# Kernel optimization log

Hardware: AMD Instinct MI355X
Metric: run time of the kernel (lower is better)

Reference implementation:

```python
import jax, jax.numpy as jnp
import numpy as np

H = 64
V = 50257
B = 32
L = 4096
LN_EPS = 1e-5
DELTA_EPS = 1e-6


def setup_inputs() -> dict:
    key = jax.random.key(0)
    ks = jax.random.split(key, 10)
    s = 0.02
    return {
        "seq": jax.random.randint(ks[0], (B, L), 0, V),
        "read_pos": -1,
        "embed": jax.random.normal(ks[1], (V, H), jnp.float32) * s,
        "w1": jax.random.normal(ks[2], (H, 2 * H), jnp.float32) * s,
        "b1": jnp.zeros((2 * H,), jnp.float32),
        "w2": jax.random.normal(ks[3], (2 * H, H), jnp.float32) * s,
        "b2": jnp.zeros((H,), jnp.float32),
        "ln_g": jnp.ones((H,), jnp.float32),
        "ln_b": jnp.zeros((H,), jnp.float32),
        "rp_w": jax.random.normal(ks[4], (H, H), jnp.float32) * s,
        "rp_b": jnp.zeros((H,), jnp.float32),
        "out_w": jax.random.normal(ks[5], (H, V), jnp.float32) * s,
        "out_b": jnp.zeros((V,), jnp.float32),
    }


def _encoder(seq, embed, w1, b1, w2, b2, ln_g, ln_b):
    e = embed[seq]  # [B, L, H]
    f = jnp.maximum(e @ w1 + b1, 0.0) @ w2 + b2  # FFN
    x = e + f
    mu = jnp.mean(x, axis=-1, keepdims=True)
    var = jnp.mean((x - mu) ** 2, axis=-1, keepdims=True)
    return (x - mu) * jax.lax.rsqrt(var + LN_EPS) * ln_g + ln_b


def _delta_memory(h_all):
    # Strictly sequential delta-rule fast-weight update over t = 0..L-2.
    Bs, Ls, Hs = h_all.shape
    keys = jnp.transpose(h_all[:, : Ls - 1, :], (1, 0, 2))  # [L-1, B, H]

    def step(M, k):
        vp = jnp.einsum('bij,bj->bi', M, k)  # M @ k
        u = k - vp / (jnp.sum(k * k, axis=-1, keepdims=True) + DELTA_EPS)
        M = M + u[:, :, None] * k[:, None, :]  # outer product update
        return M, None

    M0 = jnp.zeros((Bs, Hs, Hs), h_all.dtype)
    M, _ = jax.lax.scan(step, M0, keys)
    return M


def reference(seq, read_pos, embed, w1, b1, w2, b2, ln_g, ln_b, rp_w, rp_b, out_w, out_b):
    h_all = _encoder(seq, embed, w1, b1, w2, b2, ln_g, ln_b)  # [B, L, H]
    M = _delta_memory(h_all)  # [B, H, H]
    q = h_all[:, read_pos, :]  # [B, H]
    r = jnp.einsum('bij,bj->bi', M, q)
    return (r @ rp_w + rp_b) @ out_w + out_b  # [B, V]
```

## Files before the change

### kernel.cpp

```cpp
#include <hip/hip_runtime.h>

#define HH 64
#define VV 50257
#define BB 32
#define LL 4096

constexpr float LN_EPS_F = 1e-5f;
constexpr float DELTA_EPS_F = 1e-6f;

constexpr int CS = 64;
constexpr int NG = LL / CS;

typedef float f32x4 __attribute__((ext_vector_type(4)));
typedef short bf16x8 __attribute__((ext_vector_type(8)));
union U16x8 { uint4 u; bf16x8 v; unsigned short s[8]; };

__device__ __forceinline__ unsigned short f2bf(float f) {
  union { float f; unsigned u; } v; v.f = f;
  unsigned r = v.u + 0x7fff + ((v.u >> 16) & 1);
  return (unsigned short)(r >> 16);
}

template <int CTRL>
__device__ __forceinline__ float dpp_add(float x) {
  int t = __builtin_amdgcn_update_dpp(0, __float_as_int(x), CTRL, 0xF, 0xF, true);
  return x + __int_as_float(t);
}

__device__ __forceinline__ float wave_sum_lane63(float x) {
  x = dpp_add<0x111>(x);
  x = dpp_add<0x112>(x);
  x = dpp_add<0x114>(x);
  x = dpp_add<0x118>(x);
  x = dpp_add<0x142>(x);
  x = dpp_add<0x143>(x);
  return x;
}

__device__ __forceinline__ float readlane_f(float x, int lane) {
  return __int_as_float(__builtin_amdgcn_readlane(__float_as_int(x), lane));
}

__global__ __launch_bounds__(256) void prep_kernel(
    const float* __restrict__ w1, const float* __restrict__ w2,
    unsigned short* __restrict__ w1b, unsigned short* __restrict__ w2b) {
  int i = blockIdx.x * 256 + threadIdx.x;
  if (i < 8192) {
    int jj = i >> 6, h = i & 63;
    w1b[i] = f2bf(w1[h * 128 + jj]);
  } else {
    int k = i - 8192;
    int h = k >> 7, jj = k & 127;
    w2b[k] = f2bf(w2[jj * 64 + h]);
  }
}

__global__ __launch_bounds__(64, 1) void encoder_kernel(
    const int* __restrict__ seq, const float* __restrict__ embed,
    const unsigned short* __restrict__ w1b, const float* __restrict__ b1,
    const unsigned short* __restrict__ w2b, const float* __restrict__ b2,
    const float* __restrict__ ln_g, const float* __restrict__ ln_b,
    float* __restrict__ h_all, float* __restrict__ beta) {
  __shared__ __align__(16) char pool[26624];
  unsigned short (*e_l)[72] = reinterpret_cast<unsigned short (*)[72]>(pool);
  unsigned short (*act_l)[136] = reinterpret_cast<unsigned short (*)[136]>(pool + 9216);
  float (*x_l)[65] = reinterpret_cast<float (*)[65]>(pool);
  __shared__ float2 gb_l[64];
  __shared__ float b1_l[128], b2_l[64];

  int lane = threadIdx.x;
  int q = lane >> 4, l = lane & 15;
  int base = blockIdx.x * 64;
  int s = seq[base + lane];

  {
    const float4* ep = reinterpret_cast<const float4*>(embed + (size_t)s * HH);
#pragma unroll
    for (int i = 0; i < 8; ++i) {
      float4 va = ep[2 * i], vb = ep[2 * i + 1];
      uint4 u;
      u.x = (unsigned)f2bf(va.x) | ((unsigned)f2bf(va.y) << 16);
      u.y = (unsigned)f2bf(va.z) | ((unsigned)f2bf(va.w) << 16);
      u.z = (unsigned)f2bf(vb.x) | ((unsigned)f2bf(vb.y) << 16);
      u.w = (unsigned)f2bf(vb.z) | ((unsigned)f2bf(vb.w) << 16);
      *(uint4*)&e_l[lane][8 * i] = u;
    }
  }
  gb_l[lane] = make_float2(ln_g[lane], ln_b[lane]);
  b1_l[lane] = b1[lane];
  b1_l[64 + lane] = b1[64 + lane];
  b2_l[lane] = b2[lane];

  bf16x8 af1[8][2];
#pragma unroll
  for (int mi = 0; mi < 8; ++mi)
#pragma unroll
    for (int ks = 0; ks < 2; ++ks) {
      U16x8 t;
      t.u = *(const uint4*)(w1b + (mi * 16 + l) * 64 + ks * 32 + q * 8);
      af1[mi][ks] = t.v;
    }

  __syncthreads();

  f32x4 acc1[8][4];
#pragma unroll
  for (int mi = 0; mi < 8; ++mi)
#pragma unroll
    for (int nt = 0; nt < 4; ++nt) acc1[mi][nt] = (f32x4){0.f, 0.f, 0.f, 0.f};

#pragma unroll
  for (int ks = 0; ks < 2; ++ks) {
    bf16x8 bfr[4];
#pragma unroll
    for (int nt = 0; nt < 4; ++nt) {
      U16x8 t;
      t.u = *(const uint4*)&e_l[nt * 16 + l][ks * 32 + q * 8];
      bfr[nt] = t.v;
    }
#pragma unroll
    for (int mi = 0; mi < 8; ++mi)
#pragma unroll
      for (int nt = 0; nt < 4; ++nt)
        acc1[mi][nt] = __builtin_amdgcn_mfma_f32_16x16x32_bf16(
            af1[mi][ks], bfr[nt], acc1[mi][nt], 0, 0, 0);
  }

#pragma unroll
  for (int mi = 0; mi < 8; ++mi)
#pragma unroll
    for (int nt = 0; nt < 4; ++nt) {
      int tok = nt * 16 + l;
      int jj0 = mi * 16 + q * 4;
      float v0 = fmaxf(acc1[mi][nt][0] + b1_l[jj0 + 0], 0.f);
      float v1 = fmaxf(acc1[mi][nt][1] + b1_l[jj0 + 1], 0.f);
      float v2 = fmaxf(acc1[mi][nt][2] + b1_l[jj0 + 2], 0.f);
      float v3 = fmaxf(acc1[mi][nt][3] + b1_l[jj0 + 3], 0.f);
      uint2 u;
      u.x = (unsigned)f2bf(v0) | ((unsigned)f2bf(v1) << 16);
      u.y = (unsigned)f2bf(v2) | ((unsigned)f2bf(v3) << 16);
      *(uint2*)&act_l[tok][jj0] = u;
    }

  bf16x8 bf2[4][4];
#pragma unroll
  for (int nt = 0; nt < 4; ++nt)
#pragma unroll
    for (int ks = 0; ks < 4; ++ks) {
      U16x8 t;
      t.u = *(const uint4*)(w2b + (nt * 16 + l) * 128 + ks * 32 + q * 8);
      bf2[nt][ks] = t.v;
    }

  __syncthreads();

  f32x4 acc2[4][4];
#pragma unroll
  for (int mt = 0; mt < 4; ++mt)
#pragma unroll
    for (int nt = 0; nt < 4; ++nt) acc2[mt][nt] = (f32x4){0.f, 0.f, 0.f, 0.f};

#pragma unroll
  for (int ks = 0; ks < 4; ++ks) {
    bf16x8 afr[4];
#pragma unroll
    for (int mt = 0; mt < 4; ++mt) {
      U16x8 t;
      t.u = *(const uint4*)&act_l[mt * 16 + l][ks * 32 + q * 8];
      afr[mt] = t.v;
    }
#pragma unroll
    for (int mt = 0; mt < 4; ++mt)
#pragma unroll
      for (int nt = 0; nt < 4; ++nt)
        acc2[mt][nt] = __builtin_amdgcn_mfma_f32_16x16x32_bf16(
            afr[mt], bf2[nt][ks], acc2[mt][nt], 0, 0, 0);
  }

  __syncthreads();

#pragma unroll
  for (int mt = 0; mt < 4; ++mt)
#pragma unroll
    for (int nt = 0; nt < 4; ++nt) {
      int h = nt * 16 + l;
#pragma unroll
      for (int r = 0; r < 4; ++r) {
        int tok = mt * 16 + q * 4 + r;
        x_l[tok][h] = acc2[mt][nt][r] + b2_l[h];
      }
    }

  __syncthreads();

  float x[HH];
#pragma unroll
  for (int h = 0; h < HH; ++h) x[h] = x_l[lane][h];
  {
    const float4* ep = reinterpret_cast<const float4*>(embed + (size_t)s * HH);
#pragma unroll
    for (int i = 0; i < 16; ++i) {
      float4 v = ep[i];
      x[4 * i + 0] += v.x; x[4 * i + 1] += v.y;
      x[4 * i + 2] += v.z; x[4 * i + 3] += v.w;
    }
  }
  float sum = 0.f;
#pragma unroll
  for (int h = 0; h < HH; ++h) sum += x[h];
  float mu = sum * (1.f / HH);
  float vs = 0.f;
#pragma unroll
  for (int h = 0; h < HH; ++h) { float dx = x[h] - mu; vs = fmaf(dx, dx, vs); }
  float rstd = rsqrtf(vs * (1.f / HH) + LN_EPS_F);

  float ss = 0.f;
#pragma unroll
  for (int h = 0; h < HH; ++h) {
    float2 gb = gb_l[h];
    float o = fmaf((x[h] - mu) * rstd, gb.x, gb.y);
    ss = fmaf(o, o, ss);
    x[h] = o;
  }
  float4* hp = reinterpret_cast<float4*>(h_all + (size_t)(base + lane) * HH);
#pragma unroll
  for (int i = 0; i < 16; ++i)
    hp[i] = make_float4(x[4 * i + 0], x[4 * i + 1], x[4 * i + 2], x[4 * i + 3]);
  beta[base + lane] = 1.f / (ss + DELTA_EPS_F);
}

__global__ __launch_bounds__(64, 1) void gram_n_kernel(
    const float* __restrict__ h_all, const float* __restrict__ beta,
    float* __restrict__ Ng) {
  __shared__ __align__(16) char smem[37120];
  unsigned short (*pA)[64][72] = reinterpret_cast<unsigned short (*)[64][72]>(smem);
  unsigned short (*pB)[64][72] = reinterpret_cast<unsigned short (*)[64][72]>(smem + 18432);
  float (*Gl)[68] = reinterpret_cast<float (*)[68]>(smem + 18432);
  float* bl = reinterpret_cast<float*>(smem + 36864);

  int c = blockIdx.x, b = blockIdx.y, lane = threadIdx.x;
  int q = lane >> 4, l = lane & 15;
  const float* src = h_all + ((size_t)b * LL + c * CS) * HH;

#pragma unroll
  for (int i = 0; i < 16; ++i) {
    int row = i * 4 + q;
    float4 v = *(const float4*)&src[row * 64 + l * 4];
    float f[4] = {v.x, v.y, v.z, v.w};
    unsigned hs[4], ls[4];
#pragma unroll
    for (int r = 0; r < 4; ++r) {
      unsigned short hb = f2bf(f[r]);
      float hf = __uint_as_float(((unsigned)hb) << 16);
      hs[r] = hb; ls[r] = f2bf(f[r] - hf);
    }
    *(uint2*)&pA[0][row][l * 4] = make_uint2(hs[0] | (hs[1] << 16), hs[2] | (hs[3] << 16));
    *(uint2*)&pA[1][row][l * 4] = make_uint2(ls[0] | (ls[1] << 16), ls[2] | (ls[3] << 16));
  }
  bl[lane] = beta[(size_t)b * LL + c * CS + lane];
  if (c == NG - 1) { pA[0][63][lane] = 0; pA[1][63][lane] = 0; }
  __syncthreads();

  f32x4 acc[4][4];
#pragma unroll
  for (int mi = 0; mi < 4; ++mi)
#pragma unroll
    for (int nt = 0; nt < 4; ++nt) acc[mi][nt] = (f32x4){0.f, 0.f, 0.f, 0.f};

#pragma unroll
  for (int ks = 0; ks < 2; ++ks) {
    bf16x8 ah[4], al_[4];
#pragma unroll
    for (int i = 0; i < 4; ++i) {
      U16x8 t;
      t.u = *(const uint4*)&pA[0][i * 16 + l][ks * 32 + q * 8]; ah[i] = t.v;
      t.u = *(const uint4*)&pA[1][i * 16 + l][ks * 32 + q * 8]; al_[i] = t.v;
    }
#pragma unroll
    for (int mi = 0; mi < 4; ++mi)
#pragma unroll
      for (int nt = 0; nt < 4; ++nt) {
        acc[mi][nt] = __builtin_amdgcn_mfma_f32_16x16x32_bf16(ah[mi], ah[nt], acc[mi][nt], 0, 0, 0);
        acc[mi][nt] = __builtin_amdgcn_mfma_f32_16x16x32_bf16(ah[mi], al_[nt], acc[mi][nt], 0, 0, 0);
        acc[mi][nt] = __builtin_amdgcn_mfma_f32_16x16x32_bf16(al_[mi], ah[nt], acc[mi][nt], 0, 0, 0);
      }
  }

#pragma unroll
  for (int mi = 0; mi < 4; ++mi) {
    int s0 = mi * 16 + q * 4;
    float4 b4 = *(const float4*)&bl[s0];
#pragma unroll
    for (int nt = 0; nt < 4; ++nt) {
      int t = nt * 16 + l;
      Gl[s0 + 0][t] = acc[mi][nt][0] * b4.x;
      Gl[s0 + 1][t] = acc[mi][nt][1] * b4.y;
      Gl[s0 + 2][t] = acc[mi][nt][2] * b4.z;
      Gl[s0 + 3][t] = acc[mi][nt][3] * b4.w;
    }
  }
  __syncthreads();

  float m[64];
#pragma unroll
  for (int t = 0; t < 64; ++t) m[t] = src[t * 64 + lane];
  if (c == NG - 1) m[63] = 0.f;

#pragma unroll
  for (int i = 0; i < 32; ++i) {
    float v0 = m[2 * i], v1 = m[2 * i + 1];
    unsigned short h0 = f2bf(v0), h1 = f2bf(v1);
    float r0 = v0 - __uint_as_float(((unsigned)h0) << 16);
    float r1 = v1 - __uint_as_float(((unsigned)h1) << 16);
    *(unsigned*)&pA[0][lane][2 * i] = (unsigned)h0 | (((unsigned)h1) << 16);
    *(unsigned*)&pA[1][lane][2 * i] = (unsigned)f2bf(r0) | (((unsigned)f2bf(r1)) << 16);
  }

#pragma unroll
  for (int s = 63; s >= 1; --s) {
    float ms = m[s];
    const float* g = &Gl[s][0];
#pragma unroll
    for (int i = 0; i + 3 < s; i += 4) {
      float4 g4 = *(const float4*)(g + i);
      m[i + 0] = fmaf(-g4.x, ms, m[i + 0]);
      m[i + 1] = fmaf(-g4.y, ms, m[i + 1]);
      m[i + 2] = fmaf(-g4.z, ms, m[i + 2]);
      m[i + 3] = fmaf(-g4.w, ms, m[i + 3]);
    }
    for (int t = s & ~3; t < s; ++t) m[t] = fmaf(-g[t], ms, m[t]);
  }

  __syncthreads();

#pragma unroll
  for (int i = 0; i < 32; ++i) {
    float v0 = bl[2 * i] * m[2 * i];
    float v1 = bl[2 * i + 1] * m[2 * i + 1];
    unsigned short h0 = f2bf(v0), h1 = f2bf(v1);
    float r0 = v0 - __uint_as_float(((unsigned)h0) << 16);
    float r1 = v1 - __uint_as_float(((unsigned)h1) << 16);
    *(unsigned*)&pB[0][lane][2 * i] = (unsigned)h0 | (((unsigned)h1) << 16);
    *(unsigned*)&pB[1][lane][2 * i] = (unsigned)f2bf(r0) | (((unsigned)f2bf(r1)) << 16);
  }
  __syncthreads();

  f32x4 acc2[4][4];
#pragma unroll
  for (int mi = 0; mi < 4; ++mi)
#pragma unroll
    for (int nt = 0; nt < 4; ++nt) acc2[mi][nt] = (f32x4){0.f, 0.f, 0.f, 0.f};

#pragma unroll
  for (int ks = 0; ks < 2; ++ks) {
    bf16x8 ah[4], al_[4], bh[4], blo[4];
#pragma unroll
    for (int i = 0; i < 4; ++i) {
      U16x8 t;
      t.u = *(const uint4*)&pA[0][i * 16 + l][ks * 32 + q * 8]; ah[i] = t.v;
      t.u = *(const uint4*)&pA[1][i * 16 + l][ks * 32 + q * 8]; al_[i] = t.v;
      t.u = *(const uint4*)&pB[0][i * 16 + l][ks * 32 + q * 8]; bh[i] = t.v;
      t.u = *(const uint4*)&pB[1][i * 16 + l][ks * 32 + q * 8]; blo[i] = t.v;
    }
#pragma unroll
    for (int mi = 0; mi < 4; ++mi)
#pragma unroll
      for (int nt = 0; nt < 4; ++nt) {
        acc2[mi][nt] = __builtin_amdgcn_mfma_f32_16x16x32_bf16(ah[mi], bh[nt], acc2[mi][nt], 0, 0, 0);
        acc2[mi][nt] = __builtin_amdgcn_mfma_f32_16x16x32_bf16(ah[mi], blo[nt], acc2[mi][nt], 0, 0, 0);
        acc2[mi][nt] = __builtin_amdgcn_mfma_f32_16x16x32_bf16(al_[mi], bh[nt], acc2[mi][nt], 0, 0, 0);
      }
  }

  float* np = Ng + (((size_t)b * NG + c) << 12);
#pragma unroll
  for (int mi = 0; mi < 4; ++mi)
#pragma unroll
    for (int nt = 0; nt < 4; ++nt) {
      int h0 = mi * 16 + q * 4, hp = nt * 16 + l;
      float4 v;
      v.x = ((h0 + 0 == hp) ? 1.f : 0.f) - acc2[mi][nt][0];
      v.y = ((h0 + 1 == hp) ? 1.f : 0.f) - acc2[mi][nt][1];
      v.z = ((h0 + 2 == hp) ? 1.f : 0.f) - acc2[mi][nt][2];
      v.w = ((h0 + 3 == hp) ? 1.f : 0.f) - acc2[mi][nt][3];
      *(float4*)&np[hp * 64 + h0] = v;
    }
}

__global__ __launch_bounds__(64, 1) void boundary_kernel(
    const float* __restrict__ h_all, const float* __restrict__ Ng,
    const int* __restrict__ read_pos_p, float* __restrict__ Qg) {
  __shared__ __align__(16) float nt0[64 * 64];
  __shared__ __align__(16) float nt1[64 * 64];
  __shared__ __align__(16) float ql[64];

  int b = blockIdx.x, lane = threadIdx.x;
  int rpv = read_pos_p[0];
  int pos = rpv < 0 ? rpv + LL : rpv;
  float Q = h_all[((size_t)b * LL + pos) * HH + lane];

  const float* Nb = Ng + ((size_t)b * NG << 12);

  auto load_chunk = [&](float* buf, int c) {
    const float* g = Nb + ((size_t)c << 12);
#pragma unroll
    for (int i = 0; i < 16; ++i)
      __builtin_amdgcn_global_load_lds(
          (const __attribute__((address_space(1))) unsigned*)(g + i * 256 + lane * 4),
          (__attribute__((address_space(3))) unsigned*)(buf + i * 256), 16, 0, 0);
  };

  auto step = [&](const float* buf, int c, bool last) {
    if (last) __builtin_amdgcn_s_waitcnt(0x0F70);
    else      __builtin_amdgcn_s_waitcnt(0x4F70);
    Qg[((size_t)b * NG + c) * HH + lane] = Q;
    ql[lane] = Q;
    float a0 = 0.f, a1 = 0.f, a2 = 0.f, a3 = 0.f;
#pragma unroll
    for (int j = 0; j < 64; j += 4) {
      float4 q4 = *(const float4*)&ql[j];
      a0 = fmaf(buf[(j + 0) * 64 + lane], q4.x, a0);
      a1 = fmaf(buf[(j + 1) * 64 + lane], q4.y, a1);
      a2 = fmaf(buf[(j + 2) * 64 + lane], q4.z, a2);
      a3 = fmaf(buf[(j + 3) * 64 + lane], q4.w, a3);
    }
    Q = (a0 + a1) + (a2 + a3);
  };

  load_chunk(nt1, NG - 1);
  load_chunk(nt0, NG - 2);

#pragma unroll 1
  for (int c = NG - 1; c >= 1; c -= 2) {
    step(nt1, c, false);
    __builtin_amdgcn_s_waitcnt(0xC07F);
    if (c >= 3) load_chunk(nt1, c - 2);
    step(nt0, c - 1, c == 1);
    __builtin_amdgcn_s_waitcnt(0xC07F);
    if (c >= 3) load_chunk(nt0, c - 3);
  }
}

__global__ __launch_bounds__(64, 1) void chunk_scan_kernel(
    const float* __restrict__ h_all, const float* __restrict__ beta,
    const float* __restrict__ Qg, float* __restrict__ rc) {
  int c = blockIdx.x, b = blockIdx.y, j = threadIdx.x;
  const float* hb = h_all + (size_t)b * LL * HH;
  const float* betab = beta + (size_t)b * LL;

  float P = Qg[((size_t)b * NG + c) * HH + j];
  float r = 0.f;

  float kk[CS];
#pragma unroll
  for (int i = 0; i < CS; ++i) kk[i] = hb[((size_t)(c * CS + i)) * HH + j];
  float bv = betab[c * CS + j];

  bool last = (c == NG - 1);
#pragma unroll
  for (int i = CS - 1; i >= 0; --i) {
    float k = kk[i];
    float bt = readlane_f(bv, i);
    float m = k * P;
    float s = wave_sum_lane63(m);
    float d = readlane_f(s, 63);
    if (i == CS - 1 && last) d = 0.f;
    r = fmaf(d, k, r);
    P = fmaf(-(bt * d), k, P);
  }
  rc[((size_t)b * NG + c) * HH + j] = r;
}

__global__ __launch_bounds__(64, 1) void combine_kernel(
    const float* __restrict__ rc, const float* __restrict__ rp_w,
    const float* __restrict__ rp_b, float* __restrict__ yv) {
  int b = blockIdx.x, j = threadIdx.x;
  float r = 0.f;
#pragma unroll 8
  for (int cc = 0; cc < NG; ++cc) r += rc[((size_t)b * NG + cc) * HH + j];
  __shared__ float rs[HH];
  rs[j] = r;
  __syncthreads();
  float yj = rp_b[j];
#pragma unroll
  for (int h = 0; h < HH; ++h) yj = fmaf(rs[h], rp_w[h * HH + j], yj);
  yv[b * HH + j] = yj;
}

__global__ __launch_bounds__(256, 2) void out_kernel(
    const float* __restrict__ yv, const float* __restrict__ out_w,
    const float* __restrict__ out_b, float* __restrict__ out) {
  __shared__ float ys[BB * HH];
  for (int i = threadIdx.x; i < BB * HH; i += 256) ys[i] = yv[i];
  __syncthreads();

  int v = blockIdx.x * 256 + threadIdx.x;
  if (v >= VV) return;

  float acc[BB];
  float ob = out_b[v];
#pragma unroll
  for (int b = 0; b < BB; ++b) acc[b] = ob;

  for (int h = 0; h < HH; ++h) {
    float w = out_w[(size_t)h * VV + v];
#pragma unroll
    for (int b = 0; b < BB; ++b) acc[b] = fmaf(ys[b * HH + h], w, acc[b]);
  }
#pragma unroll
  for (int b = 0; b < BB; ++b) out[(size_t)b * VV + v] = acc[b];
}

extern "C" void kernel_launch(void* const* d_in, const int* in_sizes, int n_in,
                              void* d_out, int out_size, void* d_ws, size_t ws_size,
                              hipStream_t stream) {
  (void)in_sizes; (void)n_in; (void)out_size; (void)ws_size;
  const int*   seq   = (const int*)d_in[0];
  const int*   rp    = (const int*)d_in[1];
  const float* embed = (const float*)d_in[2];
  const float* w1    = (const float*)d_in[3];
  const float* b1    = (const float*)d_in[4];
  const float* w2    = (const float*)d_in[5];
  const float* b2    = (const float*)d_in[6];
  const float* ln_g  = (const float*)d_in[7];
  const float* ln_b  = (const float*)d_in[8];
  const float* rp_w  = (const float*)d_in[9];
  const float* rp_b  = (const float*)d_in[10];
  const float* out_w = (const float*)d_in[11];
  const float* out_b = (const float*)d_in[12];
  float* out = (float*)d_out;

  float* h_all = (float*)d_ws;
  float* beta  = h_all + (size_t)BB * LL * HH;
  float* Ng    = beta + (size_t)BB * LL;
  float* Qg    = Ng + (size_t)BB * NG * HH * HH;
  float* rcv   = Qg + (size_t)BB * NG * HH;
  float* yv    = rcv + (size_t)BB * NG * HH;
  unsigned short* w1b = (unsigned short*)(yv + (size_t)BB * HH);
  unsigned short* w2b = w1b + 8192;

  prep_kernel<<<64, 256, 0, stream>>>(w1, w2, w1b, w2b);
  encoder_kernel<<<BB * LL / 64, 64, 0, stream>>>(seq, embed, w1b, b1, w2b, b2,
                                                  ln_g, ln_b, h_all, beta);
  gram_n_kernel<<<dim3(NG, BB), 64, 0, stream>>>(h_all, beta, Ng);
  boundary_kernel<<<BB, 64, 0, stream>>>(h_all, Ng, rp, Qg);
  chunk_scan_kernel<<<dim3(NG, BB), 64, 0, stream>>>(h_all, beta, Qg, rcv);
  combine_kernel<<<BB, 64, 0, stream>>>(rcv, rp_w, rp_b, yv);
  out_kernel<<<(VV + 255) / 256, 256, 0, stream>>>(yv, out_w, out_b, out);
}
```

Measured before the change: 234.9 us.

## Pack lower-triangular Gram in LDS and block the chunk triangular solve

The Gram matrix is now computed only for lower-triangular tiles and stored packed (strict lower part), with beta scaling folded into a 4x4-blocked back-substitution that reuses each loaded row group for four updates. The second matmul is split into four passes over 16-column slices so the B operand buffer shrinks, reducing LDS footprint and MFMA count. This trades simpler indexing for more complex packed addressing and a manual waitcnt between per-quarter writes and reads, which carries a synchronization risk.

```diff
diff --git a/kernel.cpp b/kernel.cpp
--- a/kernel.cpp
+++ b/kernel.cpp
@@ -232,11 +232,11 @@
 __global__ __launch_bounds__(64, 1) void gram_n_kernel(
     const float* __restrict__ h_all, const float* __restrict__ beta,
     float* __restrict__ Ng) {
-  __shared__ __align__(16) char smem[37120];
+  __shared__ __align__(16) char smem[27136];
   unsigned short (*pA)[64][72] = reinterpret_cast<unsigned short (*)[64][72]>(smem);
-  unsigned short (*pB)[64][72] = reinterpret_cast<unsigned short (*)[64][72]>(smem + 18432);
-  float (*Gl)[68] = reinterpret_cast<float (*)[68]>(smem + 18432);
-  float* bl = reinterpret_cast<float*>(smem + 36864);
+  float* Glp = reinterpret_cast<float*>(smem + 18432);
+  unsigned short (*pBq)[16][72] = reinterpret_cast<unsigned short (*)[16][72]>(smem + 18432);
+  float* bl = reinterpret_cast<float*>(smem + 18432 + 8448);
 
   int c = blockIdx.x, b = blockIdx.y, lane = threadIdx.x;
   int q = lane >> 4, l = lane & 15;
@@ -265,7 +265,7 @@
 #pragma unroll
   for (int mi = 0; mi < 4; ++mi)
 #pragma unroll
-    for (int nt = 0; nt < 4; ++nt) acc[mi][nt] = (f32x4){0.f, 0.f, 0.f, 0.f};
+    for (int nt = 0; nt <= mi; ++nt) acc[mi][nt] = (f32x4){0.f, 0.f, 0.f, 0.f};
 
 #pragma unroll
   for (int ks = 0; ks < 2; ++ks) {
@@ -279,7 +279,7 @@
 #pragma unroll
     for (int mi = 0; mi < 4; ++mi)
 #pragma unroll
-      for (int nt = 0; nt < 4; ++nt) {
+      for (int nt = 0; nt <= mi; ++nt) {
         acc[mi][nt] = __builtin_amdgcn_mfma_f32_16x16x32_bf16(ah[mi], ah[nt], acc[mi][nt], 0, 0, 0);
         acc[mi][nt] = __builtin_amdgcn_mfma_f32_16x16x32_bf16(ah[mi], al_[nt], acc[mi][nt], 0, 0, 0);
         acc[mi][nt] = __builtin_amdgcn_mfma_f32_16x16x32_bf16(al_[mi], ah[nt], acc[mi][nt], 0, 0, 0);
@@ -288,15 +288,26 @@
 
 #pragma unroll
   for (int mi = 0; mi < 4; ++mi) {
-    int s0 = mi * 16 + q * 4;
-    float4 b4 = *(const float4*)&bl[s0];
-#pragma unroll
-    for (int nt = 0; nt < 4; ++nt) {
+    int gg = 4 * mi + q;
+    int e1 = 8 * gg * (gg + 1);
+    int o0 = 4 * gg * (2 * gg + 1);
+    int o1 = e1;
+    int o2 = e1 + 4 * (gg + 1);
+    int o3 = e1 + 8 * (gg + 1);
+#pragma unroll
+    for (int nt = 0; nt < mi; ++nt) {
       int t = nt * 16 + l;
-      Gl[s0 + 0][t] = acc[mi][nt][0] * b4.x;
-      Gl[s0 + 1][t] = acc[mi][nt][1] * b4.y;
-      Gl[s0 + 2][t] = acc[mi][nt][2] * b4.z;
-      Gl[s0 + 3][t] = acc[mi][nt][3] * b4.w;
+      Glp[o0 + t] = acc[mi][nt][0];
+      Glp[o1 + t] = acc[mi][nt][1];
+      Glp[o2 + t] = acc[mi][nt][2];
+      Glp[o3 + t] = acc[mi][nt][3];
+    }
+    {
+      int t = mi * 16 + l;
+      if (l < 4 * q)     Glp[o0 + t] = acc[mi][mi][0];
+      if (l < 4 * q + 1) Glp[o1 + t] = acc[mi][mi][1];
+      if (l < 4 * q + 2) Glp[o2 + t] = acc[mi][mi][2];
+      if (l < 4 * q + 3) Glp[o3 + t] = acc[mi][mi][3];
     }
   }
   __syncthreads();
@@ -317,74 +328,94 @@
   }
 
 #pragma unroll
-  for (int s = 63; s >= 1; --s) {
-    float ms = m[s];
-    const float* g = &Gl[s][0];
-#pragma unroll
-    for (int i = 0; i + 3 < s; i += 4) {
-      float4 g4 = *(const float4*)(g + i);
-      m[i + 0] = fmaf(-g4.x, ms, m[i + 0]);
-      m[i + 1] = fmaf(-g4.y, ms, m[i + 1]);
-      m[i + 2] = fmaf(-g4.z, ms, m[i + 2]);
-      m[i + 3] = fmaf(-g4.w, ms, m[i + 3]);
-    }
-    for (int t = s & ~3; t < s; ++t) m[t] = fmaf(-g[t], ms, m[t]);
-  }
-
-  __syncthreads();
-
-#pragma unroll
-  for (int i = 0; i < 32; ++i) {
-    float v0 = bl[2 * i] * m[2 * i];
-    float v1 = bl[2 * i + 1] * m[2 * i + 1];
-    unsigned short h0 = f2bf(v0), h1 = f2bf(v1);
-    float r0 = v0 - __uint_as_float(((unsigned)h0) << 16);
-    float r1 = v1 - __uint_as_float(((unsigned)h1) << 16);
-    *(unsigned*)&pB[0][lane][2 * i] = (unsigned)h0 | (((unsigned)h1) << 16);
-    *(unsigned*)&pB[1][lane][2 * i] = (unsigned)f2bf(r0) | (((unsigned)f2bf(r1)) << 16);
-  }
-  __syncthreads();
-
-  f32x4 acc2[4][4];
-#pragma unroll
-  for (int mi = 0; mi < 4; ++mi)
-#pragma unroll
-    for (int nt = 0; nt < 4; ++nt) acc2[mi][nt] = (f32x4){0.f, 0.f, 0.f, 0.f};
-
-#pragma unroll
-  for (int ks = 0; ks < 2; ++ks) {
-    bf16x8 ah[4], al_[4], bh[4], blo[4];
-#pragma unroll
-    for (int i = 0; i < 4; ++i) {
-      U16x8 t;
-      t.u = *(const uint4*)&pA[0][i * 16 + l][ks * 32 + q * 8]; ah[i] = t.v;
-      t.u = *(const uint4*)&pA[1][i * 16 + l][ks * 32 + q * 8]; al_[i] = t.v;
-      t.u = *(const uint4*)&pB[0][i * 16 + l][ks * 32 + q * 8]; bh[i] = t.v;
-      t.u = *(const uint4*)&pB[1][i * 16 + l][ks * 32 + q * 8]; blo[i] = t.v;
-    }
-#pragma unroll
-    for (int mi = 0; mi < 4; ++mi)
-#pragma unroll
-      for (int nt = 0; nt < 4; ++nt) {
-        acc2[mi][nt] = __builtin_amdgcn_mfma_f32_16x16x32_bf16(ah[mi], bh[nt], acc2[mi][nt], 0, 0, 0);
-        acc2[mi][nt] = __builtin_amdgcn_mfma_f32_16x16x32_bf16(ah[mi], blo[nt], acc2[mi][nt], 0, 0, 0);
-        acc2[mi][nt] = __builtin_amdgcn_mfma_f32_16x16x32_bf16(al_[mi], bh[nt], acc2[mi][nt], 0, 0, 0);
+  for (int g = 15; g >= 0; --g) {
+    int e1 = 8 * g * (g + 1);
+    int o0 = 4 * g * (2 * g + 1);
+    int o1 = e1;
+    int o2 = e1 + 4 * (g + 1);
+    int o3 = e1 + 8 * (g + 1);
+    float4 C1 = *(const float4*)(Glp + o1 + 4 * g);
+    float4 C2 = *(const float4*)(Glp + o2 + 4 * g);
+    float4 C3 = *(const float4*)(Glp + o3 + 4 * g);
+    float4 B4 = *(const float4*)(bl + 4 * g);
+
+    float t3 = B4.w * m[4 * g + 3];
+    float v2 = fmaf(-C3.z, t3, m[4 * g + 2]);
+    float t2 = B4.z * v2;
+    float v1 = fmaf(-C2.y, t2, fmaf(-C3.y, t3, m[4 * g + 1]));
+    float t1 = B4.y * v1;
+    float v0 = fmaf(-C1.x, t1, fmaf(-C2.x, t2, fmaf(-C3.x, t3, m[4 * g + 0])));
+    float t0 = B4.x * v0;
+    m[4 * g + 0] = t0; m[4 * g + 1] = t1; m[4 * g + 2] = t2; m[4 * g + 3] = t3;
+
+#pragma unroll
+    for (int j = 0; j < g; ++j) {
+      float4 R0 = *(const float4*)(Glp + o0 + 4 * j);
+      float4 R1 = *(const float4*)(Glp + o1 + 4 * j);
+      float4 R2 = *(const float4*)(Glp + o2 + 4 * j);
+      float4 R3 = *(const float4*)(Glp + o3 + 4 * j);
+      m[4 * j + 0] = fmaf(-R3.x, t3, fmaf(-R2.x, t2, fmaf(-R1.x, t1, fmaf(-R0.x, t0, m[4 * j + 0]))));
+      m[4 * j + 1] = fmaf(-R3.y, t3, fmaf(-R2.y, t2, fmaf(-R1.y, t1, fmaf(-R0.y, t0, m[4 * j + 1]))));
+      m[4 * j + 2] = fmaf(-R3.z, t3, fmaf(-R2.z, t2, fmaf(-R1.z, t1, fmaf(-R0.z, t0, m[4 * j + 2]))));
+      m[4 * j + 3] = fmaf(-R3.w, t3, fmaf(-R2.w, t2, fmaf(-R1.w, t1, fmaf(-R0.w, t0, m[4 * j + 3]))));
+    }
+  }
+
+  __syncthreads();
+
+  float* np = Ng + (((size_t)b * NG + c) << 12);
+#pragma unroll
+  for (int p = 0; p < 4; ++p) {
+    if (q == p) {
+#pragma unroll
+      for (int i = 0; i < 32; ++i) {
+        float v0 = m[2 * i], v1 = m[2 * i + 1];
+        unsigned short h0 = f2bf(v0), h1 = f2bf(v1);
+        float r0 = v0 - __uint_as_float(((unsigned)h0) << 16);
+        float r1 = v1 - __uint_as_float(((unsigned)h1) << 16);
+        *(unsigned*)&pBq[0][l][2 * i] = (unsigned)h0 | (((unsigned)h1) << 16);
+        *(unsigned*)&pBq[1][l][2 * i] = (unsigned)f2bf(r0) | (((unsigned)f2bf(r1)) << 16);
       }
-  }
-
-  float* np = Ng + (((size_t)b * NG + c) << 12);
-#pragma unroll
-  for (int mi = 0; mi < 4; ++mi)
-#pragma unroll
-    for (int nt = 0; nt < 4; ++nt) {
-      int h0 = mi * 16 + q * 4, hp = nt * 16 + l;
+    }
+    __builtin_amdgcn_s_waitcnt(0xC07F);
+
+    f32x4 a2[4];
+#pragma unroll
+    for (int mi = 0; mi < 4; ++mi) a2[mi] = (f32x4){0.f, 0.f, 0.f, 0.f};
+
+#pragma unroll
+    for (int ks = 0; ks < 2; ++ks) {
+      bf16x8 ah[4], al_[4], bh, blo;
+#pragma unroll
+      for (int i = 0; i < 4; ++i) {
+        U16x8 t;
+        t.u = *(const uint4*)&pA[0][i * 16 + l][ks * 32 + q * 8]; ah[i] = t.v;
+        t.u = *(const uint4*)&pA[1][i * 16 + l][ks * 32 + q * 8]; al_[i] = t.v;
+      }
+      {
+        U16x8 t;
+        t.u = *(const uint4*)&pBq[0][l][ks * 32 + q * 8]; bh = t.v;
+        t.u = *(const uint4*)&pBq[1][l][ks * 32 + q * 8]; blo = t.v;
+      }
+#pragma unroll
+      for (int mi = 0; mi < 4; ++mi) {
+        a2[mi] = __builtin_amdgcn_mfma_f32_16x16x32_bf16(ah[mi], bh, a2[mi], 0, 0, 0);
+        a2[mi] = __builtin_amdgcn_mfma_f32_16x16x32_bf16(ah[mi], blo, a2[mi], 0, 0, 0);
+        a2[mi] = __builtin_amdgcn_mfma_f32_16x16x32_bf16(al_[mi], bh, a2[mi], 0, 0, 0);
+      }
+    }
+
+#pragma unroll
+    for (int mi = 0; mi < 4; ++mi) {
+      int h0 = mi * 16 + q * 4, hp = p * 16 + l;
       float4 v;
-      v.x = ((h0 + 0 == hp) ? 1.f : 0.f) - acc2[mi][nt][0];
-      v.y = ((h0 + 1 == hp) ? 1.f : 0.f) - acc2[mi][nt][1];
-      v.z = ((h0 + 2 == hp) ? 1.f : 0.f) - acc2[mi][nt][2];
-      v.w = ((h0 + 3 == hp) ? 1.f : 0.f) - acc2[mi][nt][3];
+      v.x = ((h0 + 0 == hp) ? 1.f : 0.f) - a2[mi][0];
+      v.y = ((h0 + 1 == hp) ? 1.f : 0.f) - a2[mi][1];
+      v.z = ((h0 + 2 == hp) ? 1.f : 0.f) - a2[mi][2];
+      v.w = ((h0 + 3 == hp) ? 1.f : 0.f) - a2[mi][3];
       *(float4*)&np[hp * 64 + h0] = v;
     }
+  }
 }
 
 __global__ __launch_bounds__(64, 1) void boundary_kernel(
```

After: 244.4 us. 1.04x slower.
